# Optimization experiments

Measured on AMD Instinct MI355X. Metric: run time of the kernel, lower is better.

Reference implementation:

```python
import jax, jax.numpy as jnp
import numpy as np

B, S, D, H = 4, 2048, 1024, 16
DK = D // H

def setup_inputs() -> dict:
    key = jax.random.key(0)
    ks = jax.random.split(key, 7)
    f = lambda k, shape: jax.random.normal(k, shape, dtype=jnp.float32)
    return {
        "query": f(ks[0], (B, S, D)),
        "key":   f(ks[1], (B, S, D)),
        "value": f(ks[2], (B, S, D)),
        "w_q": f(ks[3], (D, D)) * (D ** -0.5),
        "w_k": f(ks[4], (D, D)) * (D ** -0.5),
        "w_v": f(ks[5], (D, D)) * (D ** -0.5),
        "w_o": f(ks[6], (D, D)) * (D ** -0.5),
    }

def reference(query, key, value, w_q, w_k, w_v, w_o):
    # Linear layers: y = x @ W^T (torch nn.Linear convention), bias=False
    def split_heads(x):  # [B,S,D] -> [B,H,S,DK]
        return x.reshape(B, S, H, DK).transpose(0, 2, 1, 3)
    Q = split_heads(query @ w_q.T)
    K = split_heads(key @ w_k.T)
    V = split_heads(value @ w_v.T)
    scale = jnp.float32(1.0 / np.sqrt(DK))
    scores = jnp.einsum('bhqd,bhkd->bhqk', Q, K) * scale  # [B,H,Sq,Sk]
    attn = jax.nn.softmax(scores, axis=-1)
    out = jnp.einsum('bhqk,bhkd->bhqd', attn, V)  # [B,H,Sq,DK]
    out = out.transpose(0, 2, 1, 3).reshape(B, S, D)
    return out @ w_o.T
```

## Files before the change

### kernel.cpp

```cpp
#include <hip/hip_runtime.h>
#include <stdint.h>

#define NB 4
#define NS 2048
#define ND 1024
#define NH 16
#define NDK 64
#define NM (NB*NS)

typedef __attribute__((ext_vector_type(8))) short short8;
typedef __attribute__((ext_vector_type(8))) unsigned short ushort8v;
typedef __attribute__((ext_vector_type(4))) unsigned short ushort4v;
typedef __attribute__((ext_vector_type(4))) float f32x4;
typedef __attribute__((ext_vector_type(16))) float f32x16;

__device__ __forceinline__ unsigned short f2bf(float f) {
  union { float f; uint32_t u; } v; v.f = f;
  uint32_t u = v.u;
  return (unsigned short)((u + 0x7FFFu + ((u >> 16) & 1u)) >> 16);
}

__device__ __forceinline__ void gload16(const void* g, void* l) {
  __builtin_amdgcn_global_load_lds(
      (const __attribute__((address_space(1))) void*)g,
      (__attribute__((address_space(3))) void*)l, 16, 0, 0);
}

__device__ __forceinline__ int xcd_swz(int flat, int nwg) {
  return (flat & 7) * (nwg >> 3) + (flat >> 3);
}

__global__ void convert_all(
    const float* __restrict__ x0, const float* __restrict__ x1, const float* __restrict__ x2,
    const float* __restrict__ w0, const float* __restrict__ w1,
    const float* __restrict__ w2, const float* __restrict__ w3,
    unsigned short* __restrict__ ox0, unsigned short* __restrict__ ox1, unsigned short* __restrict__ ox2,
    unsigned short* __restrict__ ow0, unsigned short* __restrict__ ow1,
    unsigned short* __restrict__ ow2, unsigned short* __restrict__ ow3)
{
  const float* src;
  unsigned short* dst;
  size_t i;
  if (blockIdx.y < 3) {
    src = blockIdx.y == 0 ? x0 : (blockIdx.y == 1 ? x1 : x2);
    dst = blockIdx.y == 0 ? ox0 : (blockIdx.y == 1 ? ox1 : ox2);
    i = ((size_t)blockIdx.x * 256 + threadIdx.x) * 8;
  } else {
    if (blockIdx.x >= 2048) return;
    size_t e = ((size_t)blockIdx.x * 256 + threadIdx.x) * 8;
    int which = (int)(e >> 20);
    size_t off = e & ((1u << 20) - 1);
    const float* ws[4] = {w0, w1, w2, w3};
    unsigned short* wd[4] = {ow0, ow1, ow2, ow3};
    src = ws[which]; dst = wd[which]; i = off;
  }
  f32x4 a = *(const f32x4*)(src + i);
  f32x4 b = *(const f32x4*)(src + i + 4);
  ushort8v h;
  h[0]=f2bf(a.x); h[1]=f2bf(a.y); h[2]=f2bf(a.z); h[3]=f2bf(a.w);
  h[4]=f2bf(b.x); h[5]=f2bf(b.y); h[6]=f2bf(b.z); h[7]=f2bf(b.w);
  *(ushort8v*)(dst + i) = h;
}

template<int OUT, int PRESCALE>
__device__ __forceinline__ void gemm_core(
    const unsigned short* __restrict__ A,
    const unsigned short* __restrict__ Bt,
    void* __restrict__ Cout,
    unsigned short* As, unsigned short* Bs,
    int m0, int n0)
{
  const int N = ND, K = ND;
  const int tid = threadIdx.x;
  const int lane = tid & 63, wid = tid >> 6;
  const int l15 = lane & 15, lg = lane >> 4;
  const int wr = wid >> 1, wc = wid & 1;
  const float QSC = 0.125f * 1.44269504088896f;

  f32x4 acc[4][4] = {};

  int arow[4], ach[4];
#pragma unroll
  for (int c = 0; c < 4; ++c) {
    int slot = (wid*4 + c)*64 + lane;
    arow[c] = slot >> 3; ach[c] = slot & 7;
  }

  for (int k0 = 0; k0 < K; k0 += 64) {
#pragma unroll
    for (int c = 0; c < 4; ++c) {
      gload16(A  + (size_t)(m0 + arow[c])*K + k0 + ach[c]*8, As + (wid*4 + c)*512);
      gload16(Bt + (size_t)(n0 + arow[c])*K + k0 + ach[c]*8, Bs + (wid*4 + c)*512);
    }
    __syncthreads();
#pragma unroll
    for (int kk = 0; kk < 2; ++kk) {
      short8 af[4], bfr[4];
#pragma unroll
      for (int m = 0; m < 4; ++m)
        af[m] = *(const short8*)(As + (wr*64 + m*16 + l15)*64 + kk*32 + lg*8);
#pragma unroll
      for (int n = 0; n < 4; ++n)
        bfr[n] = *(const short8*)(Bs + (wc*64 + n*16 + l15)*64 + kk*32 + lg*8);
#pragma unroll
      for (int m = 0; m < 4; ++m)
#pragma unroll
        for (int n = 0; n < 4; ++n)
          acc[m][n] = __builtin_amdgcn_mfma_f32_16x16x32_bf16(af[m], bfr[n], acc[m][n], 0, 0, 0);
    }
    __syncthreads();
  }

#pragma unroll
  for (int m = 0; m < 4; ++m)
#pragma unroll
    for (int n = 0; n < 4; ++n)
#pragma unroll
      for (int i = 0; i < 4; ++i) {
        int row = m0 + wr*64 + m*16 + lg*4 + i;
        int col = n0 + wc*64 + n*16 + l15;
        float val = PRESCALE ? acc[m][n][i] * QSC : acc[m][n][i];
        if (OUT == 0)
          ((float*)Cout)[(size_t)row * N + col] = val;
        else if (OUT == 1)
          ((unsigned short*)Cout)[(size_t)row * N + col] = f2bf(val);
        else
          ((unsigned short*)Cout)[((size_t)((row >> 11)*1024 + col))*NS + (row & (NS-1))]
              = f2bf(val);
      }
}

__global__ __launch_bounds__(256) void gemm_qkv(
    const unsigned short* __restrict__ Xq, const unsigned short* __restrict__ Wq, unsigned short* Qb,
    const unsigned short* __restrict__ Xk, const unsigned short* __restrict__ Wk, unsigned short* Kb,
    const unsigned short* __restrict__ Xv, const unsigned short* __restrict__ Wv, unsigned short* VbT)
{
  __shared__ unsigned short As[128*64];
  __shared__ unsigned short Bs[128*64];
  int flat = (blockIdx.z * 64 + blockIdx.y) * 8 + blockIdx.x;
  int swz = xcd_swz(flat, 1536);
  int z = swz >> 9, y = (swz >> 3) & 63, x = swz & 7;
  int m0 = y * 128, n0 = x * 128;
  if (z == 0)      gemm_core<1,1>(Xq, Wq, Qb,  As, Bs, m0, n0);
  else if (z == 1) gemm_core<1,0>(Xk, Wk, Kb,  As, Bs, m0, n0);
  else             gemm_core<2,0>(Xv, Wv, VbT, As, Bs, m0, n0);
}

__global__ __launch_bounds__(256) void gemm_o(
    const unsigned short* __restrict__ A, const unsigned short* __restrict__ Bt, float* C)
{
  __shared__ unsigned short As[128*64];
  __shared__ unsigned short Bs[128*64];
  int flat = blockIdx.y * 8 + blockIdx.x;
  int swz = xcd_swz(flat, 512);
  gemm_core<0,0>(A, Bt, C, As, Bs, (swz >> 3) * 128, (swz & 7) * 128);
}

__global__ __launch_bounds__(256, 4) void flash_attn(
    const unsigned short* __restrict__ Qb,
    const unsigned short* __restrict__ Kb,
    const unsigned short* __restrict__ VT,
    unsigned short* __restrict__ O)
{
  __shared__ unsigned short Kt[2][64*64];
  __shared__ unsigned short Vt[2][64*64];
  const int tid = threadIdx.x, lane = tid & 63, wid = tid >> 6;
  const int l31 = lane & 31, hi = lane >> 5;
  int flat = blockIdx.y * 16 + blockIdx.x;
  int swz = xcd_swz(flat, 1024);
  const int bh = swz >> 4, b = bh >> 4, h = bh & 15;
  const int q0 = (swz & 15) * 128 + wid * 32;

  const unsigned short* Kp[2]; const unsigned short* Vp[2]; int dofs[2];
#pragma unroll
  for (int p = 0; p < 2; ++p) {
    int slot = tid + p*256;
    int g = slot >> 6, r = slot & 63;
    Kp[p] = Kb + ((size_t)(b*NS + r))*ND + h*64 + g*8;
    Vp[p] = VT + ((size_t)(bh*64 + r))*NS + g*8;
    dofs[p] = slot * 8;
  }

  short8 qf[4];
#pragma unroll
  for (int ks = 0; ks < 4; ++ks)
    qf[ks] = *(const short8*)(Qb + (size_t)(b*NS + q0 + l31)*ND + h*64 + ks*16 + hi*8);

  f32x16 oacc[2] = {};
  float lsum = 0.f;

#pragma unroll
  for (int p = 0; p < 2; ++p) {
    gload16(Kp[p], &Kt[0][dofs[p]]);
    gload16(Vp[p], &Vt[0][dofs[p]]);
  }
  __syncthreads();

  for (int t = 0; t < NS/64; ++t) {
    const int cur = t & 1;
    if (t + 1 < NS/64) {
#pragma unroll
      for (int p = 0; p < 2; ++p) {
        gload16(Kp[p] + (size_t)(t+1)*64*ND, &Kt[cur^1][dofs[p]]);
        gload16(Vp[p] + (t+1)*64,            &Vt[cur^1][dofs[p]]);
      }
    }
    const char* Kc = (const char*)Kt[cur];
    const char* Vc = (const char*)Vt[cur];

    f32x16 st[2] = {};
    __builtin_amdgcn_s_setprio(1);
#pragma unroll
    for (int n = 0; n < 2; ++n) {
      const int r = n*32 + l31;
#pragma unroll
      for (int ks = 0; ks < 4; ++ks) {
        short8 kf = *(const short8*)(Kc + (((2*ks + hi) << 10) + r*16));
        st[n] = __builtin_amdgcn_mfma_f32_32x32x16_bf16(kf, qf[ks], st[n], 0, 0, 0);
      }
    }
    __builtin_amdgcn_s_setprio(0);

    float rs = 0.f;
#pragma unroll
    for (int n = 0; n < 2; ++n)
#pragma unroll
      for (int r = 0; r < 16; ++r) {
        float p = __builtin_amdgcn_exp2f(st[n][r]);
        st[n][r] = p;
        rs += p;
      }
    rs += __shfl_xor(rs, 32);
    lsum += rs;

    uint32_t w[2][4][2];
#pragma unroll
    for (int n = 0; n < 2; ++n)
#pragma unroll
      for (int e = 0; e < 4; ++e) {
        asm("v_cvt_pk_bf16_f32 %0, %1, %2"
            : "=v"(w[n][e][0]) : "v"(st[n][4*e+0]), "v"(st[n][4*e+1]));
        asm("v_cvt_pk_bf16_f32 %0, %1, %2"
            : "=v"(w[n][e][1]) : "v"(st[n][4*e+2]), "v"(st[n][4*e+3]));
      }

    short8 pa[2][2];
#pragma unroll
    for (int n = 0; n < 2; ++n)
#pragma unroll
      for (int ksl = 0; ksl < 2; ++ksl) {
        uint32_t a0 = w[n][2*ksl][0], b0 = w[n][2*ksl+1][0];
        uint32_t a1 = w[n][2*ksl][1], b1 = w[n][2*ksl+1][1];
        asm("v_permlane32_swap_b32 %0, %1" : "+v"(a0), "+v"(b0));
        asm("v_permlane32_swap_b32 %0, %1" : "+v"(a1), "+v"(b1));
        union { uint32_t u[4]; short8 s; } f;
        f.u[0] = a0; f.u[1] = a1; f.u[2] = b0; f.u[3] = b1;
        pa[n][ksl] = f.s;
      }

    __builtin_amdgcn_s_setprio(1);
#pragma unroll
    for (int d = 0; d < 2; ++d) {
      const int dr = d*32 + l31;
#pragma unroll
      for (int n = 0; n < 2; ++n)
#pragma unroll
        for (int ksl = 0; ksl < 2; ++ksl) {
          const int g = n*4 + ksl*2 + hi;
          short8 vf = *(const short8*)(Vc + ((g << 10) + dr*16));
          oacc[d] = __builtin_amdgcn_mfma_f32_32x32x16_bf16(pa[n][ksl], vf, oacc[d], 0, 0, 0);
        }
    }
    __builtin_amdgcn_s_setprio(0);
    __syncthreads();
  }

  float linv[16];
#pragma unroll
  for (int r = 0; r < 16; ++r)
    linv[r] = 1.0f / __shfl(lsum, (r & 3) + 8*(r >> 2) + 4*hi);
#pragma unroll
  for (int d = 0; d < 2; ++d)
#pragma unroll
    for (int r = 0; r < 16; ++r) {
      int qrow = q0 + (r & 3) + 8*(r >> 2) + 4*hi;
      O[(size_t)(b*NS + qrow)*ND + h*64 + d*32 + l31] = f2bf(oacc[d][r] * linv[r]);
    }
}

extern "C" void kernel_launch(void* const* d_in, const int* in_sizes, int n_in,
                              void* d_out, int out_size, void* d_ws, size_t ws_size,
                              hipStream_t stream) {
  const float* q  = (const float*)d_in[0];
  const float* k  = (const float*)d_in[1];
  const float* v  = (const float*)d_in[2];
  const float* wq = (const float*)d_in[3];
  const float* wk = (const float*)d_in[4];
  const float* wv = (const float*)d_in[5];
  const float* wo = (const float*)d_in[6];

  unsigned short* Wq = (unsigned short*)d_ws;
  unsigned short* Wk = Wq + (size_t)ND*ND;
  unsigned short* Wv = Wk + (size_t)ND*ND;
  unsigned short* Wo = Wv + (size_t)ND*ND;
  unsigned short* Xq = Wo + (size_t)ND*ND;
  unsigned short* Xk = Xq + (size_t)NM*ND;
  unsigned short* Xv = Xk + (size_t)NM*ND;
  unsigned short* Qb = Xv + (size_t)NM*ND;
  unsigned short* Kb = Qb + (size_t)NM*ND;
  unsigned short* VbT = (unsigned short*)d_out;
  unsigned short* Ob  = Xq;

  convert_all<<<dim3(NM*ND/(256*8), 4), 256, 0, stream>>>(
      q, k, v, wq, wk, wv, wo, Xq, Xk, Xv, Wq, Wk, Wv, Wo);

  gemm_qkv<<<dim3(8, 64, 3), 256, 0, stream>>>(Xq, Wq, Qb, Xk, Wk, Kb, Xv, Wv, VbT);

  flash_attn<<<dim3(16, 64), 256, 0, stream>>>(Qb, Kb, VbT, Ob);

  gemm_o<<<dim3(8, 64), 256, 0, stream>>>(Ob, Wo, (float*)d_out);
}
```

Before: 227.2 us.

## Rewrite projection GEMMs with 256x256 tiles, double-buffered LDS, and swizzled layout

Replaces the 128x128 single-buffered GEMM used by the QKV and output projections with a 256x256-tile, 512-thread kernel. It double-buffers LDS so global loads of the next K slice overlap MFMA work, XOR-swizzles LDS columns to avoid bank conflicts, and splits the compute into phases with barriers and s_setprio. The goal is more operand reuse per byte loaded and hidden load latency. The cost is 128 KB of LDS per block, more registers, and far fewer blocks (128 for gemm_o), which can leave compute units idle on a 256-CU part.

```diff
diff --git a/kernel.cpp b/kernel.cpp
--- a/kernel.cpp
+++ b/kernel.cpp
@@ -62,62 +62,100 @@
   *(ushort8v*)(dst + i) = h;
 }
 
+#define GPHASE(MH, NH, LA, LB)                                                 \
+  {                                                                            \
+    if (LA) {                                                                  \
+      _Pragma("unroll") for (int mm = 0; mm < 4; ++mm)                         \
+        _Pragma("unroll") for (int kk = 0; kk < 2; ++kk)                       \
+          af[mm][kk] = *(const short8*)(Ab + (MH)*8192 + mm*2048 + rowb + aoff[kk]); \
+    }                                                                          \
+    if (LB) {                                                                  \
+      _Pragma("unroll") for (int nn = 0; nn < 2; ++nn)                         \
+        _Pragma("unroll") for (int kk = 0; kk < 2; ++kk)                       \
+          bf[nn][kk] = *(const short8*)(Bb + (NH)*4096 + nn*2048 + rowb + aoff[kk]); \
+    }                                                                          \
+    __builtin_amdgcn_s_barrier();                                              \
+    __builtin_amdgcn_s_setprio(1);                                             \
+    _Pragma("unroll") for (int mm = 0; mm < 4; ++mm)                           \
+      _Pragma("unroll") for (int nn = 0; nn < 2; ++nn)                         \
+        _Pragma("unroll") for (int kk = 0; kk < 2; ++kk)                       \
+          acc[(MH)*4+mm][(NH)*2+nn] = __builtin_amdgcn_mfma_f32_16x16x32_bf16( \
+              af[mm][kk], bf[nn][kk], acc[(MH)*4+mm][(NH)*2+nn], 0, 0, 0);     \
+    __builtin_amdgcn_s_setprio(0);                                             \
+    __builtin_amdgcn_s_barrier();                                              \
+  }
+
 template<int OUT, int PRESCALE>
-__device__ __forceinline__ void gemm_core(
+__device__ __forceinline__ void gemm256_core(
     const unsigned short* __restrict__ A,
     const unsigned short* __restrict__ Bt,
     void* __restrict__ Cout,
-    unsigned short* As, unsigned short* Bs,
-    int m0, int n0)
-{
-  const int N = ND, K = ND;
+    unsigned short* lds, int m0, int n0)
+{
+  const int K = ND, N = ND;
   const int tid = threadIdx.x;
   const int lane = tid & 63, wid = tid >> 6;
   const int l15 = lane & 15, lg = lane >> 4;
-  const int wr = wid >> 1, wc = wid & 1;
+  const int wr = wid >> 2, wc = wid & 3;
   const float QSC = 0.125f * 1.44269504088896f;
 
-  f32x4 acc[4][4] = {};
-
-  int arow[4], ach[4];
-#pragma unroll
-  for (int c = 0; c < 4; ++c) {
-    int slot = (wid*4 + c)*64 + lane;
-    arow[c] = slot >> 3; ach[c] = slot & 7;
-  }
-
-  for (int k0 = 0; k0 < K; k0 += 64) {
-#pragma unroll
-    for (int c = 0; c < 4; ++c) {
-      gload16(A  + (size_t)(m0 + arow[c])*K + k0 + ach[c]*8, As + (wid*4 + c)*512);
-      gload16(Bt + (size_t)(n0 + arow[c])*K + k0 + ach[c]*8, Bs + (wid*4 + c)*512);
-    }
-    __syncthreads();
-#pragma unroll
-    for (int kk = 0; kk < 2; ++kk) {
-      short8 af[4], bfr[4];
-#pragma unroll
-      for (int m = 0; m < 4; ++m)
-        af[m] = *(const short8*)(As + (wr*64 + m*16 + l15)*64 + kk*32 + lg*8);
-#pragma unroll
-      for (int n = 0; n < 4; ++n)
-        bfr[n] = *(const short8*)(Bs + (wc*64 + n*16 + l15)*64 + kk*32 + lg*8);
-#pragma unroll
-      for (int m = 0; m < 4; ++m)
-#pragma unroll
-        for (int n = 0; n < 4; ++n)
-          acc[m][n] = __builtin_amdgcn_mfma_f32_16x16x32_bf16(af[m], bfr[n], acc[m][n], 0, 0, 0);
-    }
-    __syncthreads();
-  }
-
-#pragma unroll
-  for (int m = 0; m < 4; ++m)
+  const unsigned short* Asrc[4];
+  const unsigned short* Bsrc[4];
+#pragma unroll
+  for (int l = 0; l < 4; ++l) {
+    int cidx = l*512 + tid;
+    int r = cidx >> 3;
+    int cs = ((cidx & 7) ^ (r & 7)) * 8;
+    Asrc[l] = A  + (size_t)(m0 + r)*K + cs;
+    Bsrc[l] = Bt + (size_t)(n0 + r)*K + cs;
+  }
+
+  const int rowb = l15 * 128;
+  int aoff[2];
+  aoff[0] = ((lg)     ^ (l15 & 7)) * 16;
+  aoff[1] = ((4 + lg) ^ (l15 & 7)) * 16;
+
+  f32x4 acc[8][4] = {};
+  short8 af[4][2], bf[2][2];
+
+#pragma unroll
+  for (int l = 0; l < 4; ++l) {
+    gload16(Asrc[l], lds + l*4096 + tid*8);
+    gload16(Bsrc[l], lds + 16384 + l*4096 + tid*8);
+  }
+  asm volatile("s_waitcnt vmcnt(0)" ::: "memory");
+  __builtin_amdgcn_s_barrier();
+
+  const int NT = K / 64;
+  for (int t = 0; t < NT; ++t) {
+    const int cur = t & 1;
+    if (t + 1 < NT) {
+      unsigned short* dstA = lds + (cur^1)*32768;
+#pragma unroll
+      for (int l = 0; l < 4; ++l) {
+        gload16(Asrc[l] + (t+1)*64, dstA + l*4096 + tid*8);
+        gload16(Bsrc[l] + (t+1)*64, dstA + 16384 + l*4096 + tid*8);
+      }
+    }
+    const char* Ab = (const char*)(lds + cur*32768) + wr*16384;
+    const char* Bb = (const char*)(lds + cur*32768 + 16384) + (wc>>1)*16384 + (wc&1)*8192;
+
+    GPHASE(0, 0, 1, 1)
+    GPHASE(0, 1, 0, 1)
+    GPHASE(1, 1, 1, 0)
+    GPHASE(1, 0, 0, 1)
+
+    asm volatile("s_waitcnt vmcnt(0)" ::: "memory");
+    __builtin_amdgcn_s_barrier();
+  }
+
+#pragma unroll
+  for (int m = 0; m < 8; ++m)
 #pragma unroll
     for (int n = 0; n < 4; ++n)
 #pragma unroll
       for (int i = 0; i < 4; ++i) {
-        int row = m0 + wr*64 + m*16 + lg*4 + i;
+        int row = m0 + wr*128 + m*16 + lg*4 + i;
         int col = n0 + wc*64 + n*16 + l15;
         float val = PRESCALE ? acc[m][n][i] * QSC : acc[m][n][i];
         if (OUT == 0)
@@ -130,30 +168,28 @@
       }
 }
 
-__global__ __launch_bounds__(256) void gemm_qkv(
+__global__ __launch_bounds__(512, 2) void gemm_qkv(
     const unsigned short* __restrict__ Xq, const unsigned short* __restrict__ Wq, unsigned short* Qb,
     const unsigned short* __restrict__ Xk, const unsigned short* __restrict__ Wk, unsigned short* Kb,
     const unsigned short* __restrict__ Xv, const unsigned short* __restrict__ Wv, unsigned short* VbT)
 {
-  __shared__ unsigned short As[128*64];
-  __shared__ unsigned short Bs[128*64];
-  int flat = (blockIdx.z * 64 + blockIdx.y) * 8 + blockIdx.x;
-  int swz = xcd_swz(flat, 1536);
-  int z = swz >> 9, y = (swz >> 3) & 63, x = swz & 7;
-  int m0 = y * 128, n0 = x * 128;
-  if (z == 0)      gemm_core<1,1>(Xq, Wq, Qb,  As, Bs, m0, n0);
-  else if (z == 1) gemm_core<1,0>(Xk, Wk, Kb,  As, Bs, m0, n0);
-  else             gemm_core<2,0>(Xv, Wv, VbT, As, Bs, m0, n0);
-}
-
-__global__ __launch_bounds__(256) void gemm_o(
+  __shared__ unsigned short lds[65536];
+  int flat = (blockIdx.z * 32 + blockIdx.y) * 4 + blockIdx.x;
+  int swz = xcd_swz(flat, 384);
+  int z = swz >> 7, rem = swz & 127;
+  int m0 = (rem >> 2) * 256, n0 = (rem & 3) * 256;
+  if (z == 0)      gemm256_core<1,1>(Xq, Wq, Qb,  lds, m0, n0);
+  else if (z == 1) gemm256_core<1,0>(Xk, Wk, Kb,  lds, m0, n0);
+  else             gemm256_core<2,0>(Xv, Wv, VbT, lds, m0, n0);
+}
+
+__global__ __launch_bounds__(512, 2) void gemm_o(
     const unsigned short* __restrict__ A, const unsigned short* __restrict__ Bt, float* C)
 {
-  __shared__ unsigned short As[128*64];
-  __shared__ unsigned short Bs[128*64];
-  int flat = blockIdx.y * 8 + blockIdx.x;
-  int swz = xcd_swz(flat, 512);
-  gemm_core<0,0>(A, Bt, C, As, Bs, (swz >> 3) * 128, (swz & 7) * 128);
+  __shared__ unsigned short lds[65536];
+  int flat = blockIdx.y * 4 + blockIdx.x;
+  int swz = xcd_swz(flat, 128);
+  gemm256_core<0,0>(A, Bt, C, lds, (swz >> 2) * 256, (swz & 3) * 256);
 }
 
 __global__ __launch_bounds__(256, 4) void flash_attn(
@@ -314,9 +350,9 @@
   convert_all<<<dim3(NM*ND/(256*8), 4), 256, 0, stream>>>(
       q, k, v, wq, wk, wv, wo, Xq, Xk, Xv, Wq, Wk, Wv, Wo);
 
-  gemm_qkv<<<dim3(8, 64, 3), 256, 0, stream>>>(Xq, Wq, Qb, Xk, Wk, Kb, Xv, Wv, VbT);
+  gemm_qkv<<<dim3(4, 32, 3), 512, 0, stream>>>(Xq, Wq, Qb, Xk, Wk, Kb, Xv, Wv, VbT);
 
   flash_attn<<<dim3(16, 64), 256, 0, stream>>>(Qb, Kb, VbT, Ob);
 
-  gemm_o<<<dim3(8, 64), 256, 0, stream>>>(Ob, Wo, (float*)d_out);
-}
+  gemm_o<<<dim3(4, 32), 512, 0, stream>>>(Ob, Wo, (float*)d_out);
+}
```

Result: faster. 220.0 us (-3.1%).
